# Optimization experiments

Hardware: AMD Instinct MI355X
Metric: run time of the kernel (lower is better)

## Reference

```python
import jax, jax.numpy as jnp
import numpy as np

B, S, D, H = 2, 2048, 1024, 16
DK = D // H

def setup_inputs() -> dict:
    key = jax.random.key(0)
    ks = jax.random.split(key, 5)
    std = 1.0 / np.sqrt(D)
    return {
        "x": jax.random.normal(ks[0], (B, S, D), dtype=jnp.float32),
        "wq": jax.random.normal(ks[1], (D, D), dtype=jnp.float32) * std,
        "wk": jax.random.normal(ks[2], (D, D), dtype=jnp.float32) * std,
        "wv": jax.random.normal(ks[3], (D, D), dtype=jnp.float32) * std,
        "wo": jax.random.normal(ks[4], (D, D), dtype=jnp.float32) * std,
    }

def reference(x, wq, wk, wv, wo):
    b, s, d = x.shape
    # torch Linear(bias=False): x @ W.T
    q = (x @ wq.T).reshape(b, s, H, DK).transpose(0, 2, 1, 3)  # [b,h,s,dk]
    k = (x @ wk.T).reshape(b, s, H, DK).transpose(0, 2, 1, 3)
    v = (x @ wv.T).reshape(b, s, H, DK).transpose(0, 2, 1, 3)
    scale = jnp.sqrt(jnp.asarray(DK, dtype=x.dtype))
    scores = jnp.einsum('bhqd,bhkd->bhqk', q, k) / scale  # [b,h,s,s]
    # causal mask (masking=True): lower-triangular kept, rest -inf
    causal = jnp.tril(jnp.ones((s, s), dtype=bool))
    scores = jnp.where(causal[None, None], scores, -jnp.inf)
    attn = jax.nn.softmax(scores, axis=-1)
    out = jnp.einsum('bhqk,bhkd->bhqd', attn, v)  # [b,h,s,dk]
    out = out.transpose(0, 2, 1, 3).reshape(b, s, d)
    return out @ wo.T
```

## Files before the change

kernel.cpp:

```cpp
#include <hip/hip_runtime.h>

#define LB __launch_bounds__(256)

typedef __bf16 bf16x8 __attribute__((ext_vector_type(8)));
typedef float f32x4 __attribute__((ext_vector_type(4)));
typedef float f32x16 __attribute__((ext_vector_type(16)));
typedef unsigned int u32;
typedef unsigned int u32x2 __attribute__((ext_vector_type(2)));

constexpr int B = 2, S = 2048, D = 1024, H = 16, DK = 64;
constexpr int M = B * S;
constexpr int K = D;

__device__ __forceinline__ unsigned short f2bf(float f) {
    union { float f; unsigned u; } v; v.f = f;
    unsigned r = v.u + 0x7fffu + ((v.u >> 16) & 1u);
    return (unsigned short)(r >> 16);
}

__device__ __forceinline__ u32 pk2bf(float lo, float hi) {
    union { __bf16 h[2]; u32 w; } u;
    u.h[0] = (__bf16)lo; u.h[1] = (__bf16)hi;
    return u.w;
}

__device__ __forceinline__ void gld_lds16(const unsigned short* g, unsigned short* l) {
    __builtin_amdgcn_global_load_lds(
        (const __attribute__((address_space(1))) unsigned int*)g,
        (__attribute__((address_space(3))) unsigned int*)l, 16, 0, 0);
}

__global__ LB void cvt_all(const float* __restrict__ x,  const float* __restrict__ wq,
                           const float* __restrict__ wk, const float* __restrict__ wv,
                           const float* __restrict__ wo, unsigned short* __restrict__ dst) {
    const size_t NX = (size_t)M * D;
    const size_t NW = (size_t)D * D;
    size_t i = ((size_t)blockIdx.x * 256 + threadIdx.x) * 4;
    if (i >= NX + 4 * NW) return;
    const float* src; size_t off;
    if      (i < NX)          { src = x;  off = i; }
    else if (i < NX + NW)     { src = wq; off = i - NX; }
    else if (i < NX + 2 * NW) { src = wk; off = i - NX - NW; }
    else if (i < NX + 3 * NW) { src = wv; off = i - NX - 2 * NW; }
    else                      { src = wo; off = i - NX - 3 * NW; }
    float4 f = *reinterpret_cast<const float4*>(src + off);
    ushort4 o;
    o.x = f2bf(f.x); o.y = f2bf(f.y); o.z = f2bf(f.z); o.w = f2bf(f.w);
    *reinterpret_cast<ushort4*>(dst + i) = o;
}

__global__ LB void gemm_qkv(const unsigned short* __restrict__ A,
                            const unsigned short* __restrict__ wqb,
                            const unsigned short* __restrict__ wkb,
                            const unsigned short* __restrict__ wvb,
                            unsigned short* __restrict__ qo,
                            unsigned short* __restrict__ ko,
                            unsigned short* __restrict__ vo) {
    __shared__ __align__(16) unsigned short lA[128 * 32];
    __shared__ __align__(16) unsigned short lB[128 * 32];
    const int z = blockIdx.y;
    const unsigned short* W = (z == 0) ? wqb : ((z == 1) ? wkb : wvb);
    int bid = blockIdx.x;
    int m0 = (((bid >> 6) << 3) | (bid & 7)) * 128;
    int n0 = ((bid >> 3) & 7) * 128;
    int t = threadIdx.x;
    int w = t >> 6, lane = t & 63;
    int r = lane & 15, g = lane >> 4;
    int wr = w >> 1, wc = w & 1;
    int rowT = t >> 2, colOff = (t & 3) * 8;

    f32x4 acc[4][4];
#pragma unroll
    for (int mi = 0; mi < 4; ++mi)
#pragma unroll
        for (int ni = 0; ni < 4; ++ni) acc[mi][ni] = f32x4{0.f, 0.f, 0.f, 0.f};

    for (int k0 = 0; k0 < K; k0 += 32) {
        gld_lds16(A + (size_t)(m0 + rowT) * K + k0 + colOff,      lA + (w * 64) * 8);
        gld_lds16(A + (size_t)(m0 + 64 + rowT) * K + k0 + colOff, lA + (256 + w * 64) * 8);
        gld_lds16(W + (size_t)(n0 + rowT) * K + k0 + colOff,      lB + (w * 64) * 8);
        gld_lds16(W + (size_t)(n0 + 64 + rowT) * K + k0 + colOff, lB + (256 + w * 64) * 8);
        __syncthreads();
        bf16x8 af[4], bfr[4];
#pragma unroll
        for (int mi = 0; mi < 4; ++mi)
            af[mi] = *reinterpret_cast<const bf16x8*>(&lA[(wr * 64 + mi * 16 + r) * 32 + g * 8]);
#pragma unroll
        for (int ni = 0; ni < 4; ++ni)
            bfr[ni] = *reinterpret_cast<const bf16x8*>(&lB[(wc * 64 + ni * 16 + r) * 32 + g * 8]);
#pragma unroll
        for (int mi = 0; mi < 4; ++mi)
#pragma unroll
            for (int ni = 0; ni < 4; ++ni)
                acc[mi][ni] = __builtin_amdgcn_mfma_f32_16x16x32_bf16(af[mi], bfr[ni], acc[mi][ni], 0, 0, 0);
        __syncthreads();
    }

    const float QSCALE = 0.125f * 1.44269504088896341f;
    float scale = (z == 0) ? QSCALE : 1.0f;
    unsigned short* dst = (z == 0) ? qo : ((z == 1) ? ko : vo);
#pragma unroll
    for (int mi = 0; mi < 4; ++mi)
#pragma unroll
        for (int ni = 0; ni < 4; ++ni)
#pragma unroll
            for (int j = 0; j < 4; ++j) {
                int row = m0 + wr * 64 + mi * 16 + g * 4 + j;
                int col = n0 + wc * 64 + ni * 16 + r;
                int b = row >> 11, s = row & (S - 1);
                int h = col >> 6, dk = col & 63;
                size_t bh = (size_t)(b * H + h);
                unsigned short val = f2bf(acc[mi][ni][j] * scale);
                if (z == 0) {
                    dst[(bh * S + s) * DK + dk] = val;
                } else if (z == 1) {
                    int kt32 = s >> 5, q5k = s & 31;
                    int dsi = dk >> 4, hlk = (dk >> 3) & 1, e = dk & 7;
                    dst[(((bh * 64 + kt32) * 4 + dsi) * 64 + (hlk * 32 + q5k)) * 8 + e] = val;
                } else {
                    int ktile = s >> 6, ks2 = (s >> 4) & 3, hlv = (s >> 3) & 1, e = s & 7;
                    int rh = dk >> 5, q5r = dk & 31;
                    dst[(((bh * 32 + ktile) * 8 + rh * 4 + ks2) * 64 + (hlv * 32 + q5r)) * 8 + e] = val;
                }
            }
}

__global__ LB void out_gemm(const unsigned short* __restrict__ A,
                            const unsigned short* __restrict__ W,
                            float* __restrict__ out) {
    __shared__ __align__(16) unsigned short lA[128 * 32];
    __shared__ __align__(16) unsigned short lB[64 * 32];
    int bid = blockIdx.x;
    int m0 = (((bid >> 7) << 3) | (bid & 7)) * 128;
    int n0 = ((bid >> 3) & 15) * 64;
    int t = threadIdx.x;
    int w = t >> 6, lane = t & 63;
    int r = lane & 15, g = lane >> 4;
    int wr = w >> 1, wc = w & 1;
    int rowT = t >> 2, colOff = (t & 3) * 8;

    f32x4 acc[4][2];
#pragma unroll
    for (int mi = 0; mi < 4; ++mi)
#pragma unroll
        for (int ni = 0; ni < 2; ++ni) acc[mi][ni] = f32x4{0.f, 0.f, 0.f, 0.f};

    for (int k0 = 0; k0 < K; k0 += 32) {
        gld_lds16(A + (size_t)(m0 + rowT) * K + k0 + colOff,      lA + (w * 64) * 8);
        gld_lds16(A + (size_t)(m0 + 64 + rowT) * K + k0 + colOff, lA + (256 + w * 64) * 8);
        gld_lds16(W + (size_t)(n0 + rowT) * K + k0 + colOff,      lB + (w * 64) * 8);
        __syncthreads();
        bf16x8 af[4], bfr[2];
#pragma unroll
        for (int mi = 0; mi < 4; ++mi)
            af[mi] = *reinterpret_cast<const bf16x8*>(&lA[(wr * 64 + mi * 16 + r) * 32 + g * 8]);
#pragma unroll
        for (int ni = 0; ni < 2; ++ni)
            bfr[ni] = *reinterpret_cast<const bf16x8*>(&lB[(wc * 32 + ni * 16 + r) * 32 + g * 8]);
#pragma unroll
        for (int mi = 0; mi < 4; ++mi)
#pragma unroll
            for (int ni = 0; ni < 2; ++ni)
                acc[mi][ni] = __builtin_amdgcn_mfma_f32_16x16x32_bf16(af[mi], bfr[ni], acc[mi][ni], 0, 0, 0);
        __syncthreads();
    }

#pragma unroll
    for (int mi = 0; mi < 4; ++mi)
#pragma unroll
        for (int ni = 0; ni < 2; ++ni)
#pragma unroll
            for (int j = 0; j < 4; ++j) {
                int row = m0 + wr * 64 + mi * 16 + g * 4 + j;
                int col = n0 + wc * 32 + ni * 16 + r;
                out[(size_t)row * D + col] = acc[mi][ni][j];
            }
}

__global__ __launch_bounds__(64) void flash_attn(
        const unsigned short* __restrict__ q,
        const unsigned short* __restrict__ kmat,
        const unsigned short* __restrict__ vt,
        unsigned short* __restrict__ ao) {
    int bid = blockIdx.x;
    int kk = bid >> 8, cc = bid & 255;
    int r9 = (kk << 8) | ((kk & 1) ? (255 - cc) : cc);
    int qt = 63 - (r9 >> 5);
    int bh = r9 & 31;
    int b = bh >> 4, hd = bh & 15;
    int q0 = qt << 5;
    int nt = (qt + 2) >> 1;

    int l = threadIdx.x;
    int q5 = l & 31, hl = l >> 5;
    int qglob = q0 + q5;

    const unsigned short* qp = q    + (size_t)bh * S * DK;
    const unsigned short* kf = kmat + (size_t)bh * S * DK;
    const unsigned short* vf = vt   + (size_t)bh * S * DK;

    bf16x8 ones;
#pragma unroll
    for (int i = 0; i < 8; ++i) ones[i] = (__bf16)1.0f;

    const f32x16 z16 = {0,0,0,0,0,0,0,0,0,0,0,0,0,0,0,0};

    bf16x8 qf[4];
#pragma unroll
    for (int dsi = 0; dsi < 4; ++dsi)
        qf[dsi] = *reinterpret_cast<const bf16x8*>(qp + (size_t)qglob * DK + dsi * 16 + hl * 8);

    f32x16 acc0 = z16, acc1 = z16, accl = z16;

    auto loadK = [&](bf16x8 (&kr)[8], int kb) {
        const unsigned short* base = kf + (size_t)(kb >> 5) * 4 * 512 + l * 8;
#pragma unroll
        for (int dsi = 0; dsi < 4; ++dsi) {
            kr[dsi]     = *reinterpret_cast<const bf16x8*>(base + dsi * 512);
            kr[4 + dsi] = *reinterpret_cast<const bf16x8*>(base + (4 + dsi) * 512);
        }
    };
    auto loadV = [&](bf16x8 (&vr)[8], int kb) {
        const unsigned short* base = vf + (size_t)(kb >> 6) * 8 * 512 + l * 8;
#pragma unroll
        for (int i2 = 0; i2 < 8; ++i2)
            vr[i2] = *reinterpret_cast<const bf16x8*>(base + i2 * 512);
    };
    auto compute = [&](bf16x8 (&kr)[8], bf16x8 (&vr)[8], int kb) {
        f32x16 st0 = __builtin_amdgcn_mfma_f32_32x32x16_bf16(kr[0], qf[0], z16, 0, 0, 0);
        f32x16 st1 = __builtin_amdgcn_mfma_f32_32x32x16_bf16(kr[4], qf[0], z16, 0, 0, 0);
#pragma unroll
        for (int dsi = 1; dsi < 4; ++dsi) {
            st0 = __builtin_amdgcn_mfma_f32_32x32x16_bf16(kr[dsi],     qf[dsi], st0, 0, 0, 0);
            st1 = __builtin_amdgcn_mfma_f32_32x32x16_bf16(kr[4 + dsi], qf[dsi], st1, 0, 0, 0);
        }
        if (kb + 31 > q0) {
#pragma unroll
            for (int r = 0; r < 16; ++r) {
                int kv = kb + (r & 3) + 8 * (r >> 2) + 4 * hl;
                st0[r] = (kv <= qglob) ? st0[r] : -1e30f;
            }
        }
        if (kb + 63 > q0) {
#pragma unroll
            for (int r = 0; r < 16; ++r) {
                int kv = kb + 32 + (r & 3) + 8 * (r >> 2) + 4 * hl;
                st1[r] = (kv <= qglob) ? st1[r] : -1e30f;
            }
        }
#pragma unroll
        for (int r = 0; r < 16; ++r) { st0[r] = exp2f(st0[r]); st1[r] = exp2f(st1[r]); }
        u32 pk[2][8];
#pragma unroll
        for (int rg = 0; rg < 4; ++rg) {
            pk[0][2*rg]   = pk2bf(st0[4*rg],   st0[4*rg+1]);
            pk[0][2*rg+1] = pk2bf(st0[4*rg+2], st0[4*rg+3]);
            pk[1][2*rg]   = pk2bf(st1[4*rg],   st1[4*rg+1]);
            pk[1][2*rg+1] = pk2bf(st1[4*rg+2], st1[4*rg+3]);
        }
        union PF { bf16x8 vv; u32 w[4]; } pf[4];
#pragma unroll
        for (int ti2 = 0; ti2 < 2; ++ti2)
#pragma unroll
            for (int s = 0; s < 2; ++s) {
                u32x2 r0 = __builtin_amdgcn_permlane32_swap(pk[ti2][4*s],   pk[ti2][4*s+2], false, false);
                u32x2 r1 = __builtin_amdgcn_permlane32_swap(pk[ti2][4*s+1], pk[ti2][4*s+3], false, false);
                PF f;
                f.w[0] = r0[0]; f.w[1] = r1[0];
                f.w[2] = r0[1]; f.w[3] = r1[1];
                pf[ti2*2+s] = f;
            }
#pragma unroll
        for (int ks = 0; ks < 4; ++ks) {
            acc0 = __builtin_amdgcn_mfma_f32_32x32x16_bf16(vr[ks],     pf[ks].vv, acc0, 0, 0, 0);
            acc1 = __builtin_amdgcn_mfma_f32_32x32x16_bf16(vr[4 + ks], pf[ks].vv, acc1, 0, 0, 0);
            accl = __builtin_amdgcn_mfma_f32_32x32x16_bf16(ones,       pf[ks].vv, accl, 0, 0, 0);
        }
    };

    bf16x8 ka[8], kb2[8], va[8], vb2[8];
    loadK(ka, 0);
    loadV(va, 0);
    int it = 0;
    while (true) {
        if (it + 1 < nt) { loadK(kb2, (it + 1) << 6); loadV(vb2, (it + 1) << 6); }
        compute(ka, va, it << 6);
        ++it; if (it >= nt) break;
        if (it + 1 < nt) { loadK(ka, (it + 1) << 6); loadV(va, (it + 1) << 6); }
        compute(kb2, vb2, it << 6);
        ++it; if (it >= nt) break;
    }

    float inv = 1.0f / accl[0];
    size_t obase = ((size_t)(b * S + qglob)) * D + hd * DK;
#pragma unroll
    for (int rg = 0; rg < 4; ++rg) {
        uint2 wd;
        wd.x = pk2bf(acc0[4*rg]   * inv, acc0[4*rg+1] * inv);
        wd.y = pk2bf(acc0[4*rg+2] * inv, acc0[4*rg+3] * inv);
        *reinterpret_cast<uint2*>(ao + obase + rg * 8 + hl * 4) = wd;
        uint2 we;
        we.x = pk2bf(acc1[4*rg]   * inv, acc1[4*rg+1] * inv);
        we.y = pk2bf(acc1[4*rg+2] * inv, acc1[4*rg+3] * inv);
        *reinterpret_cast<uint2*>(ao + obase + 32 + rg * 8 + hl * 4) = we;
    }
}

extern "C" void kernel_launch(void* const* d_in, const int* in_sizes, int n_in,
                              void* d_out, int out_size, void* d_ws, size_t ws_size,
                              hipStream_t stream) {
    const float* x  = (const float*)d_in[0];
    const float* wq = (const float*)d_in[1];
    const float* wk = (const float*)d_in[2];
    const float* wv = (const float*)d_in[3];
    const float* wo = (const float*)d_in[4];
    char* ws = (char*)d_ws;
    unsigned short* xb  = (unsigned short*)(ws);
    unsigned short* wqb = (unsigned short*)(ws + (size_t)(8  << 20));
    unsigned short* wkb = (unsigned short*)(ws + (size_t)(10 << 20));
    unsigned short* wvb = (unsigned short*)(ws + (size_t)(12 << 20));
    unsigned short* wob = (unsigned short*)(ws + (size_t)(14 << 20));
    unsigned short* qb  = (unsigned short*)(ws + (size_t)(16 << 20));
    unsigned short* kb  = (unsigned short*)(ws + (size_t)(24 << 20));
    unsigned short* vtb = (unsigned short*)(ws + (size_t)(32 << 20));
    unsigned short* aob = (unsigned short*)(ws + (size_t)(40 << 20));

    cvt_all<<<8192, 256, 0, stream>>>(x, wq, wk, wv, wo, xb);

    gemm_qkv<<<dim3(256, 3), 256, 0, stream>>>(xb, wqb, wkb, wvb, qb, kb, vtb);
    flash_attn<<<2048, 64, 0, stream>>>(qb, kb, vtb, aob);
    out_gemm<<<512, 256, 0, stream>>>(aob, wob, (float*)d_out);
}
```

Baseline: 114.1 us.

## Split causal attention key range into two halves and merge partial outputs

```diff
diff --git a/kernel.cpp b/kernel.cpp
--- a/kernel.cpp
+++ b/kernel.cpp
@@ -22,6 +22,11 @@
     union { __bf16 h[2]; u32 w; } u;
     u.h[0] = (__bf16)lo; u.h[1] = (__bf16)hi;
     return u.w;
+}
+
+__device__ __forceinline__ float bf2f(unsigned short h) {
+    union { unsigned u; float f; } v; v.u = ((unsigned)h) << 16;
+    return v.f;
 }
 
 __device__ __forceinline__ void gld_lds16(const unsigned short* g, unsigned short* l) {
@@ -181,15 +186,23 @@
         const unsigned short* __restrict__ q,
         const unsigned short* __restrict__ kmat,
         const unsigned short* __restrict__ vt,
-        unsigned short* __restrict__ ao) {
+        unsigned short* __restrict__ p0,
+        unsigned short* __restrict__ p1,
+        float* __restrict__ l0,
+        float* __restrict__ l1) {
     int bid = blockIdx.x;
-    int kk = bid >> 8, cc = bid & 255;
-    int r9 = (kk << 8) | ((kk & 1) ? (255 - cc) : cc);
-    int qt = 63 - (r9 >> 5);
-    int bh = r9 & 31;
+    int qt = 63 - (bid >> 6);
+    int half = (bid >> 5) & 1;
+    int bh = bid & 31;
     int b = bh >> 4, hd = bh & 15;
     int q0 = qt << 5;
     int nt = (qt + 2) >> 1;
+    int nh1 = (nt + 1) >> 1;
+    int n_lo = half ? nh1 : 0;
+    int n_hi = half ? nt : nh1;
+
+    unsigned short* Pd = half ? p1 : p0;
+    float* Ld = half ? l1 : l0;
 
     int l = threadIdx.x;
     int q5 = l & 31, hl = l >> 5;
@@ -279,31 +292,61 @@
     };
 
     bf16x8 ka[8], kb2[8], va[8], vb2[8];
-    loadK(ka, 0);
-    loadV(va, 0);
-    int it = 0;
-    while (true) {
-        if (it + 1 < nt) { loadK(kb2, (it + 1) << 6); loadV(vb2, (it + 1) << 6); }
-        compute(ka, va, it << 6);
-        ++it; if (it >= nt) break;
-        if (it + 1 < nt) { loadK(ka, (it + 1) << 6); loadV(va, (it + 1) << 6); }
-        compute(kb2, vb2, it << 6);
-        ++it; if (it >= nt) break;
+    int it = n_lo;
+    if (it < n_hi) {
+        loadK(ka, it << 6);
+        loadV(va, it << 6);
+        while (true) {
+            if (it + 1 < n_hi) { loadK(kb2, (it + 1) << 6); loadV(vb2, (it + 1) << 6); }
+            compute(ka, va, it << 6);
+            ++it; if (it >= n_hi) break;
+            if (it + 1 < n_hi) { loadK(ka, (it + 1) << 6); loadV(va, (it + 1) << 6); }
+            compute(kb2, vb2, it << 6);
+            ++it; if (it >= n_hi) break;
+        }
     }
 
-    float inv = 1.0f / accl[0];
+    if (hl == 0) Ld[(size_t)bh * S + q0 + q5] = accl[0];
     size_t obase = ((size_t)(b * S + qglob)) * D + hd * DK;
 #pragma unroll
     for (int rg = 0; rg < 4; ++rg) {
         uint2 wd;
-        wd.x = pk2bf(acc0[4*rg]   * inv, acc0[4*rg+1] * inv);
-        wd.y = pk2bf(acc0[4*rg+2] * inv, acc0[4*rg+3] * inv);
-        *reinterpret_cast<uint2*>(ao + obase + rg * 8 + hl * 4) = wd;
+        wd.x = pk2bf(acc0[4*rg],   acc0[4*rg+1]);
+        wd.y = pk2bf(acc0[4*rg+2], acc0[4*rg+3]);
+        *reinterpret_cast<uint2*>(Pd + obase + rg * 8 + hl * 4) = wd;
         uint2 we;
-        we.x = pk2bf(acc1[4*rg]   * inv, acc1[4*rg+1] * inv);
-        we.y = pk2bf(acc1[4*rg+2] * inv, acc1[4*rg+3] * inv);
-        *reinterpret_cast<uint2*>(ao + obase + 32 + rg * 8 + hl * 4) = we;
+        we.x = pk2bf(acc1[4*rg],   acc1[4*rg+1]);
+        we.y = pk2bf(acc1[4*rg+2], acc1[4*rg+3]);
+        *reinterpret_cast<uint2*>(Pd + obase + 32 + rg * 8 + hl * 4) = we;
     }
+}
+
+__global__ LB void merge_o(unsigned short* __restrict__ p0,
+                           const unsigned short* __restrict__ p1,
+                           const float* __restrict__ l0,
+                           const float* __restrict__ l1) {
+    size_t i = ((size_t)blockIdx.x * 256 + threadIdx.x) * 8;
+    int row = (int)(i >> 10);
+    int col = (int)(i & 1023);
+    int h = col >> 6;
+    int b = row >> 11, s = row & (S - 1);
+    size_t bh = (size_t)(b * H + h);
+    float inv = 1.0f / (l0[bh * S + s] + l1[bh * S + s]);
+    ushort4 a0 = *reinterpret_cast<const ushort4*>(p0 + i);
+    ushort4 a1 = *reinterpret_cast<const ushort4*>(p0 + i + 4);
+    ushort4 b0 = *reinterpret_cast<const ushort4*>(p1 + i);
+    ushort4 b1 = *reinterpret_cast<const ushort4*>(p1 + i + 4);
+    ushort4 o0, o1;
+    o0.x = f2bf((bf2f(a0.x) + bf2f(b0.x)) * inv);
+    o0.y = f2bf((bf2f(a0.y) + bf2f(b0.y)) * inv);
+    o0.z = f2bf((bf2f(a0.z) + bf2f(b0.z)) * inv);
+    o0.w = f2bf((bf2f(a0.w) + bf2f(b0.w)) * inv);
+    o1.x = f2bf((bf2f(a1.x) + bf2f(b1.x)) * inv);
+    o1.y = f2bf((bf2f(a1.y) + bf2f(b1.y)) * inv);
+    o1.z = f2bf((bf2f(a1.z) + bf2f(b1.z)) * inv);
+    o1.w = f2bf((bf2f(a1.w) + bf2f(b1.w)) * inv);
+    *reinterpret_cast<ushort4*>(p0 + i)     = o0;
+    *reinterpret_cast<ushort4*>(p0 + i + 4) = o1;
 }
 
 extern "C" void kernel_launch(void* const* d_in, const int* in_sizes, int n_in,
@@ -323,11 +366,15 @@
     unsigned short* qb  = (unsigned short*)(ws + (size_t)(16 << 20));
     unsigned short* kb  = (unsigned short*)(ws + (size_t)(24 << 20));
     unsigned short* vtb = (unsigned short*)(ws + (size_t)(32 << 20));
-    unsigned short* aob = (unsigned short*)(ws + (size_t)(40 << 20));
+    unsigned short* p0  = (unsigned short*)(ws + (size_t)(40 << 20));
+    unsigned short* p1  = (unsigned short*)(ws);
+    float* l0 = (float*)(ws + (size_t)(8 << 20));
+    float* l1 = (float*)(ws + (size_t)(9 << 20));
 
     cvt_all<<<8192, 256, 0, stream>>>(x, wq, wk, wv, wo, xb);
 
     gemm_qkv<<<dim3(256, 3), 256, 0, stream>>>(xb, wqb, wkb, wvb, qb, kb, vtb);
-    flash_attn<<<2048, 64, 0, stream>>>(qb, kb, vtb, aob);
-    out_gemm<<<512, 256, 0, stream>>>(aob, wob, (float*)d_out);
-}
+    flash_attn<<<4096, 64, 0, stream>>>(qb, kb, vtb, p0, p1, l0, l1);
+    merge_o<<<2048, 256, 0, stream>>>(p0, p1, l0, l1);
+    out_gemm<<<512, 256, 0, stream>>>(p0, wob, (float*)d_out);
+}
```

Result: slower. 120.1 us (+5.3%).
